# Kernel tuning notes

Hardware: AMD Instinct MI355X
Metric: run time of the kernel (lower is better)

Reference implementation:

```python
import jax, jax.numpy as jnp
import numpy as np

M_DIM = 1024
N_HEADS = 16
H_DIM = M_DIM // N_HEADS
B, S_DEC, S_ENC = 2, 2048, 2048
NEG = -1e9
LN_EPS = 1e-5


def _layernorm(x, g, b):
    mu = jnp.mean(x, axis=-1, keepdims=True)
    var = jnp.mean(jnp.square(x - mu), axis=-1, keepdims=True)
    return (x - mu) * jax.lax.rsqrt(var + LN_EPS) * g + b


def _mha(q_in, kv_in, Wq, bq, Wk, bk, Wv, bv, causal):
    # Wq/Wk/Wv: [H, m_dim, h_dim]; stacked equivalent of per-head nn.Linear
    q = jnp.einsum('bsm,hmd->bhsd', q_in, Wq) + bq[:, None, :]
    k = jnp.einsum('bsm,hmd->bhsd', kv_in, Wk) + bk[:, None, :]
    v = jnp.einsum('bsm,hmd->bhsd', kv_in, Wv) + bv[:, None, :]
    scores = jnp.einsum('bhqd,bhkd->bhqk', q, k) / jnp.sqrt(jnp.asarray(H_DIM, q.dtype))
    if causal:
        sq, sk = scores.shape[-2], scores.shape[-1]
        mask = jnp.tril(jnp.ones((sq, sk), dtype=bool))
        scores = jnp.where(mask, scores, jnp.asarray(NEG, scores.dtype))
    attn = jax.nn.softmax(scores, axis=-1)
    o = jnp.einsum('bhqk,bhkd->bhqd', attn, v)
    bsz, h, sq, d = o.shape
    # concat order: head-major along last dim, same as torch.cat over heads
    return o.transpose(0, 2, 1, 3).reshape(bsz, sq, h * d)


def setup_inputs() -> dict:
    key = jax.random.key(0)
    ks = jax.random.split(key, 32)
    s = 1.0 / np.sqrt(M_DIM)
    s2 = 1.0 / np.sqrt(2 * M_DIM)
    d = {
        'input': jax.random.normal(ks[0], (B, S_DEC, M_DIM), jnp.float32),
        'encoder_out': jax.random.normal(ks[1], (B, S_ENC, M_DIM), jnp.float32),
        # self-attention heads (stacked)
        'Wq1': jax.random.normal(ks[2], (N_HEADS, M_DIM, H_DIM), jnp.float32) * s,
        'bq1': jnp.zeros((N_HEADS, H_DIM), jnp.float32),
        'Wk1': jax.random.normal(ks[3], (N_HEADS, M_DIM, H_DIM), jnp.float32) * s,
        'bk1': jnp.zeros((N_HEADS, H_DIM), jnp.float32),
        'Wv1': jax.random.normal(ks[4], (N_HEADS, M_DIM, H_DIM), jnp.float32) * s,
        'bv1': jnp.zeros((N_HEADS, H_DIM), jnp.float32),
        'Wo1': jax.random.normal(ks[5], (M_DIM, M_DIM), jnp.float32) * s,
        'bo1': jnp.zeros((M_DIM,), jnp.float32),
        'ln1_g': jnp.ones((M_DIM,), jnp.float32),
        'ln1_b': jnp.zeros((M_DIM,), jnp.float32),
        # cross-attention heads (stacked)
        'Wq2': jax.random.normal(ks[6], (N_HEADS, M_DIM, H_DIM), jnp.float32) * s,
        'bq2': jnp.zeros((N_HEADS, H_DIM), jnp.float32),
        'Wk2': jax.random.normal(ks[7], (N_HEADS, M_DIM, H_DIM), jnp.float32) * s,
        'bk2': jnp.zeros((N_HEADS, H_DIM), jnp.float32),
        'Wv2': jax.random.normal(ks[8], (N_HEADS, M_DIM, H_DIM), jnp.float32) * s,
        'bv2': jnp.zeros((N_HEADS, H_DIM), jnp.float32),
        'Wo2': jax.random.normal(ks[9], (M_DIM, M_DIM), jnp.float32) * s,
        'bo2': jnp.zeros((M_DIM,), jnp.float32),
        'ln2_g': jnp.ones((M_DIM,), jnp.float32),
        'ln2_b': jnp.zeros((M_DIM,), jnp.float32),
        # FFN (expansion factor 2, per source)
        'W_ff1': jax.random.normal(ks[10], (M_DIM, 2 * M_DIM), jnp.float32) * s,
        'b_ff1': jnp.zeros((2 * M_DIM,), jnp.float32),
        'W_ff2': jax.random.normal(ks[11], (2 * M_DIM, M_DIM), jnp.float32) * s2,
        'b_ff2': jnp.zeros((M_DIM,), jnp.float32),
        'ln3_g': jnp.ones((M_DIM,), jnp.float32),
        'ln3_b': jnp.zeros((M_DIM,), jnp.float32),
    }
    return d


def reference(input, encoder_out,
              Wq1, bq1, Wk1, bk1, Wv1, bv1, Wo1, bo1, ln1_g, ln1_b,
              Wq2, bq2, Wk2, bk2, Wv2, bv2, Wo2, bo2, ln2_g, ln2_b,
              W_ff1, b_ff1, W_ff2, b_ff2, ln3_g, ln3_b):
    # masked self-attention (dropout = identity in eval)
    sa = _mha(input, input, Wq1, bq1, Wk1, bk1, Wv1, bv1, causal=True)
    sa = sa @ Wo1 + bo1
    out1 = _layernorm(sa + input, ln1_g, ln1_b)
    # cross-attention
    ca = _mha(out1, encoder_out, Wq2, bq2, Wk2, bk2, Wv2, bv2, causal=False)
    ca = ca @ Wo2 + bo2
    out1 = _layernorm(out1 + ca, ln2_g, ln2_b)
    # FFN
    ff = jax.nn.relu(out1 @ W_ff1 + b_ff1) @ W_ff2 + b_ff2
    out = _layernorm(ff + out1, ln3_g, ln3_b)
    return out
```

## Files before the change

kernel.cpp:

```cpp
#include <hip/hip_runtime.h>
#include <math.h>

#define B_ 2
#define S_ 2048
#define M_ 1024
#define H_ 16
#define D_ 64
#define R_ (B_*S_)

typedef __attribute__((ext_vector_type(8))) short short8v;
typedef __attribute__((ext_vector_type(4))) float float4v;
typedef __attribute__((ext_vector_type(16))) float float16v;

__device__ __forceinline__ float4 ld4(const float* p) {
    return *(const float4* __restrict__)p;
}

__device__ __forceinline__ ushort f2bf(float f) {
    union { float f; unsigned u; } x; x.f = f;
    unsigned u = x.u + 0x7fffu + ((x.u >> 16) & 1u);
    return (ushort)(u >> 16);
}
__device__ __forceinline__ float bf2f(ushort s) {
    union { unsigned u; float f; } x; x.u = ((unsigned)s) << 16; return x.f;
}
__device__ __forceinline__ unsigned cvtpk(float lo, float hi) {
    unsigned r;
    asm("v_cvt_pk_bf16_f32 %0, %1, %2" : "=v"(r) : "v"(lo), "v"(hi));
    return r;
}
#if __has_builtin(__builtin_amdgcn_exp2f)
__device__ __forceinline__ float fexp2(float x) { return __builtin_amdgcn_exp2f(x); }
#else
__device__ __forceinline__ float fexp2(float x) { return exp2f(x); }
#endif
#if __has_builtin(__builtin_amdgcn_rcpf)
__device__ __forceinline__ float frcp(float x) { return __builtin_amdgcn_rcpf(x); }
#else
__device__ __forceinline__ float frcp(float x) { return 1.f / x; }
#endif
__device__ __forceinline__ float4v mfma16(short8v a, short8v b, float4v c) {
    return __builtin_amdgcn_mfma_f32_16x16x32_bf16(a, b, c, 0, 0, 0);
}
__device__ __forceinline__ float16v mfma32(short8v a, short8v b, float16v c) {
    return __builtin_amdgcn_mfma_f32_32x32x16_bf16(a, b, c, 0, 0, 0);
}
__device__ __forceinline__ void glds16(const void* g, void* l) {
    __builtin_amdgcn_global_load_lds(
        (const __attribute__((address_space(1))) void*)g,
        (__attribute__((address_space(3))) void*)l, 16, 0, 0);
}

__global__ __launch_bounds__(256) void cast2_k(const float* __restrict__ a,
                                               const float* __restrict__ b,
                                               ushort* __restrict__ oa,
                                               ushort* __restrict__ ob) {
    size_t u = (size_t)blockIdx.x * 256 + threadIdx.x;
    const float* in; ushort* out;
    if (u < (1u << 20)) { in = a; out = oa; }
    else { u -= (1u << 20); in = b; out = ob; }
    float4 v = ld4(in + u * 4);
    ushort4 o = { f2bf(v.x), f2bf(v.y), f2bf(v.z), f2bf(v.w) };
    *(ushort4*)&out[u * 4] = o;
}

__global__ __launch_bounds__(256) void biasp_k(
    const float* __restrict__ q1, const float* __restrict__ k1,
    const float* __restrict__ v1, const float* __restrict__ k2,
    const float* __restrict__ v2, const float* __restrict__ q2,
    float* __restrict__ dst, float SCv) {
    const int seg = blockIdx.x >> 2;
    const int li = (blockIdx.x & 3) * 256 + threadIdx.x;
    const float* s; int off; float sc;
    switch (seg) {
        case 0: s = q1; off = 0;    sc = SCv; break;
        case 1: s = k1; off = 1024; sc = 1.f; break;
        case 2: s = v1; off = 2048; sc = 1.f; break;
        case 3: s = k2; off = 4096; sc = 1.f; break;
        case 4: s = v2; off = 5120; sc = 1.f; break;
        default: s = q2; off = 8192; sc = SCv; break;
    }
    dst[off + li] = s[li] * sc;
}

__global__ __launch_bounds__(256) void wtransH_k(
    const float* __restrict__ s0, const float* __restrict__ s1,
    const float* __restrict__ s2, const float* __restrict__ s3,
    const float* __restrict__ s4, const float* __restrict__ s5,
    ushort* __restrict__ oQKV1, ushort* __restrict__ oQ2,
    ushort* __restrict__ oKV2, float SCv) {
    __shared__ float t[32][33];
    const int z = blockIdx.z, s6 = z >> 4, h = z & 15;
    const float* srcs[6] = { s0, s1, s2, s3, s4, s5 };
    const float* ib = srcs[s6] + (size_t)h * 1024 * 64;
    ushort* ob;
    if (s6 < 3)       ob = oQKV1 + (size_t)s6 * (1024 * 1024) + (size_t)h * (64 * 1024);
    else if (s6 == 3) ob = oQ2 + (size_t)h * (64 * 1024);
    else              ob = oKV2 + (size_t)(s6 - 4) * (1024 * 1024) + (size_t)h * (64 * 1024);
    const float scale = (s6 == 0 || s6 == 3) ? SCv : 1.f;
    const int k0 = blockIdx.y * 32, n0 = blockIdx.x * 32;
    const int tx = threadIdx.x & 31, ty = threadIdx.x >> 5;
    #pragma unroll
    for (int i = 0; i < 4; ++i)
        t[ty + i * 8][tx] = ib[(size_t)(k0 + ty + i * 8) * 64 + n0 + tx];
    __syncthreads();
    #pragma unroll
    for (int i = 0; i < 4; ++i)
        ob[(size_t)(n0 + ty + i * 8) * 1024 + k0 + tx] = f2bf(t[tx][ty + i * 8] * scale);
}

__global__ __launch_bounds__(256) void wtrans_k(const float* __restrict__ inA,
                                                const float* __restrict__ inB,
                                                ushort* __restrict__ outA,
                                                ushort* __restrict__ outB,
                                                int K, int N) {
    __shared__ float t[32][33];
    const float* ib = blockIdx.z ? inB : inA;
    ushort* ob = blockIdx.z ? outB : outA;
    const int k0 = blockIdx.y * 32, n0 = blockIdx.x * 32;
    const int tx = threadIdx.x & 31, ty = threadIdx.x >> 5;
    #pragma unroll
    for (int i = 0; i < 4; ++i)
        t[ty + i * 8][tx] = ib[(size_t)(k0 + ty + i * 8) * N + n0 + tx];
    __syncthreads();
    #pragma unroll
    for (int i = 0; i < 4; ++i)
        ob[(size_t)(n0 + ty + i * 8) * K + k0 + tx] = f2bf(t[tx][ty + i * 8]);
}

template<int TM, int TN, int BK, int OUTMODE, int ACT>
__global__ __launch_bounds__(256) void gemm_bf16_k(
    const ushort* __restrict__ A, const ushort* __restrict__ Bt,
    const float* __restrict__ bias, void* __restrict__ C,
    ushort* __restrict__ Cvt, int matV, int N, int K)
{
    constexpr int NI = TM / 32;
    constexpr int NJ = TN / 32;
    constexpr int KS = BK / 32;
    constexpr int CHR = BK / 8;
    __shared__ __align__(16) ushort At[TM * BK];
    __shared__ __align__(16) ushort Bts[TN * BK];
    const int tid = threadIdx.x, lane = tid & 63, w = tid >> 6;
    const int wm = w >> 1, wn = w & 1;
    const int q = lane & 15, g = lane >> 4;
    const int m0 = blockIdx.y * TM, n0 = blockIdx.x * TN;

    float4v acc[NI][NJ];
    #pragma unroll
    for (int i = 0; i < NI; ++i)
        #pragma unroll
        for (int j = 0; j < NJ; ++j) acc[i][j] = (float4v){0.f, 0.f, 0.f, 0.f};

    for (int k0 = 0; k0 < K; k0 += BK) {
        #pragma unroll
        for (int t = 0; t < TM * CHR / 256; ++t) {
            const int cb = (w * (TM * CHR / 256) + t) * 64;
            const int c = cb + lane;
            const int row = c / CHR, kc = (c % CHR) ^ (row & (CHR - 1));
            glds16(&A[(size_t)(m0 + row) * K + k0 + kc * 8], &At[cb * 8]);
        }
        #pragma unroll
        for (int t = 0; t < TN * CHR / 256; ++t) {
            const int cb = (w * (TN * CHR / 256) + t) * 64;
            const int c = cb + lane;
            const int row = c / CHR, kc = (c % CHR) ^ (row & (CHR - 1));
            glds16(&Bt[(size_t)(n0 + row) * K + k0 + kc * 8], &Bts[cb * 8]);
        }
        __syncthreads();
        #pragma unroll
        for (int ks = 0; ks < KS; ++ks) {
            short8v af[NI], bf[NJ];
            #pragma unroll
            for (int i = 0; i < NI; ++i) {
                const int row = wm * (TM / 2) + i * 16 + q;
                af[i] = *(const short8v*)((const char*)At +
                        row * (BK * 2) + (((ks * 4 + g) ^ (q & (CHR - 1))) << 4));
            }
            #pragma unroll
            for (int j = 0; j < NJ; ++j) {
                const int row = wn * (TN / 2) + j * 16 + q;
                bf[j] = *(const short8v*)((const char*)Bts +
                        row * (BK * 2) + (((ks * 4 + g) ^ (q & (CHR - 1))) << 4));
            }
            #pragma unroll
            for (int i = 0; i < NI; ++i)
                #pragma unroll
                for (int j = 0; j < NJ; ++j)
                    acc[i][j] = mfma16(af[i], bf[j], acc[i][j]);
        }
        __syncthreads();
    }

    float bcol[NJ];
    #pragma unroll
    for (int j = 0; j < NJ; ++j) bcol[j] = bias[n0 + wn * (TN / 2) + j * 16 + q];

    #pragma unroll
    for (int i = 0; i < NI; ++i) {
        const int rowg0 = m0 + wm * (TM / 2) + i * 16 + g * 4;
        #pragma unroll
        for (int j = 0; j < NJ; ++j) {
            const int colg = n0 + wn * (TN / 2) + j * 16 + q;
            float v[4];
            #pragma unroll
            for (int r = 0; r < 4; ++r) {
                v[r] = acc[i][j][r] + bcol[j];
                if (ACT) v[r] = fmaxf(v[r], 0.f);
            }
            if (OUTMODE == 0) {
                #pragma unroll
                for (int r = 0; r < 4; ++r)
                    ((float*)C)[(size_t)(rowg0 + r) * N + colg] = v[r];
            } else if (OUTMODE == 1) {
                #pragma unroll
                for (int r = 0; r < 4; ++r)
                    ((ushort*)C)[(size_t)(rowg0 + r) * N + colg] = f2bf(v[r]);
            } else {
                const int mat = colg >> 10, h = (colg >> 6) & 15, d = colg & 63;
                const int bb = rowg0 >> 11, s0 = rowg0 & 2047;
                if (mat == matV) {
                    uint2 pv;
                    pv.x = cvtpk(v[0], v[1]);
                    pv.y = cvtpk(v[2], v[3]);
                    *(uint2*)&Cvt[((size_t)(bb * H_ + h) * D_ + d) * S_ + s0] = pv;
                } else {
                    #pragma unroll
                    for (int r = 0; r < 4; ++r)
                        ((ushort*)C)[((((size_t)(mat * B_ + bb) * H_ + h) * S_) + s0 + r) * D_ + d] = f2bf(v[r]);
                }
            }
        }
    }
}

template<int CAUSAL>
__global__ __launch_bounds__(256, 3) void fattn_k(
    const ushort* __restrict__ Qg, const ushort* __restrict__ Kg,
    const ushort* __restrict__ VTg, ushort* __restrict__ Og, int Skv)
{
    __shared__ __align__(16) ushort Kt[2][64 * 64];
    __shared__ __align__(16) ushort Vt[2][64 * 64];
    const int tid = threadIdx.x, lane = tid & 63, w = tid >> 6;
    const int q = lane & 31, hi = lane >> 5;
    const int id = blockIdx.x;
    const int bh = id & 31;
    const int t_ = id >> 5;
    const int qb = CAUSAL ? ((t_ < 8) ? (15 - t_) : (t_ - 8)) : t_;
    const int q0b = qb * 128;
    const int q0w = q0b + w * 32;
    const float MB = 24.f;

    const int c0 = tid, c1 = tid + 256;
    const ushort* kS0 = Kg + ((size_t)bh * Skv + (c0 >> 3)) * 64 + (((c0 & 7) ^ ((c0 >> 3) & 7)) * 8);
    const ushort* kS1 = Kg + ((size_t)bh * Skv + (c1 >> 3)) * 64 + (((c1 & 7) ^ ((c1 >> 3) & 7)) * 8);
    const ushort* vS0 = VTg + ((size_t)bh * 64 + (c0 >> 3)) * (size_t)Skv + (((c0 & 7) ^ ((c0 >> 3) & 7)) * 8);
    const ushort* vS1 = VTg + ((size_t)bh * 64 + (c1 >> 3)) * (size_t)Skv + (((c1 & 7) ^ ((c1 >> 3) & 7)) * 8);

#define STAGE(nb) do { \
        glds16(kS0, &Kt[nb][(w * 64) * 8]); \
        glds16(kS1, &Kt[nb][(256 + w * 64) * 8]); \
        glds16(vS0, &Vt[nb][(w * 64) * 8]); \
        glds16(vS1, &Vt[nb][(256 + w * 64) * 8]); \
        kS0 += 64 * 64; kS1 += 64 * 64; vS0 += 64; vS1 += 64; } while (0)

    short8v qf[4];
    #pragma unroll
    for (int ki = 0; ki < 4; ++ki)
        qf[ki] = *(const short8v*)&Qg[((size_t)bh * S_ + q0w + q) * 64 + ki * 16 + hi * 8];

    const int ktB = q * 128 + ((hi ^ (q & 7)) << 4);

    float16v oacc0, oacc1;
    #pragma unroll
    for (int r = 0; r < 16; ++r) { oacc0[r] = 0.f; oacc1[r] = 0.f; }
    float l_ = 0.f;

    const int ktiles = CAUSAL ? (2 * qb + 2) : (Skv >> 6);
    int cur = 0;

    STAGE(0);
    __syncthreads();

    for (int kt = 0; kt < ktiles; ++kt) {
        if (kt + 1 < ktiles) STAGE(cur ^ 1);
        const char* ktp = (const char*)Kt + cur * 8192;
        const char* vtp = (const char*)Vt + cur * 8192;
        const int kv0 = kt * 64;

        float16v st0, st1;
        #pragma unroll
        for (int r = 0; r < 16; ++r) { st0[r] = 0.f; st1[r] = 0.f; }
        __builtin_amdgcn_s_setprio(1);
        #pragma unroll
        for (int ki = 0; ki < 4; ++ki) {
            short8v kf0 = *(const short8v*)(ktp + (ktB ^ (ki << 5)));
            short8v kf1 = *(const short8v*)(ktp + (ktB ^ (ki << 5)) + 4096);
            st0 = mfma32(kf0, qf[ki], st0);
            st1 = mfma32(kf1, qf[ki], st1);
        }
        __builtin_amdgcn_s_setprio(0);

        if (CAUSAL && kv0 + 63 > q0b) {
            const int qg_ = q0w + q;
            #pragma unroll
            for (int r = 0; r < 16; ++r) {
                const int row = (r & 3) + 8 * (r >> 2) + 4 * hi;
                if (kv0 + row > qg_)      st0[r] = -1e9f;
                if (kv0 + 32 + row > qg_) st1[r] = -1e9f;
            }
        }

        float ts[16];
        #pragma unroll
        for (int r = 0; r < 16; ++r) {
            st0[r] = fexp2(st0[r] - MB);
            st1[r] = fexp2(st1[r] - MB);
            ts[r] = st0[r] + st1[r];
        }
        #pragma unroll
        for (int off = 8; off >= 1; off >>= 1)
            #pragma unroll
            for (int i = 0; i < 8; ++i)
                if (i < off) ts[i] += ts[i + off];
        l_ += ts[0] + __shfl_xor(ts[0], 32);

        unsigned W0[8], W1[8];
        #pragma unroll
        for (int s = 0; s < 8; ++s) {
            W0[s] = cvtpk(st0[2 * s], st0[2 * s + 1]);
            W1[s] = cvtpk(st1[2 * s], st1[2 * s + 1]);
        }

        short8v bq[4];
        #pragma unroll
        for (int kb = 0; kb < 4; ++kb) {
            union { unsigned u[4]; short8v v; } bb;
            #pragma unroll
            for (int j = 0; j < 4; ++j) {
                const unsigned* Wb = (kb >> 1) ? W1 : W0;
                const int s0 = (j & 1) + 4 * (kb & 1);
                const unsigned own  = hi ? Wb[s0 + 2] : Wb[s0];
                const unsigned send = hi ? Wb[s0]     : Wb[s0 + 2];
                const unsigned rec  = (unsigned)__shfl_xor((int)send, 32);
                bb.u[j] = (j >> 1) ? (hi ? own : rec) : (hi ? rec : own);
            }
            bq[kb] = bb.v;
        }

        __builtin_amdgcn_s_setprio(1);
        #pragma unroll
        for (int kb = 0; kb < 4; ++kb) {
            short8v vf0 = *(const short8v*)(vtp + (ktB ^ (kb << 5)));
            short8v vf1 = *(const short8v*)(vtp + (ktB ^ (kb << 5)) + 4096);
            oacc0 = mfma32(vf0, bq[kb], oacc0);
            oacc1 = mfma32(vf1, bq[kb], oacc1);
        }
        __builtin_amdgcn_s_setprio(0);

        __syncthreads();
        cur ^= 1;
    }
#undef STAGE

    float lr = l_ + __shfl_xor(l_, 32) - __shfl_xor(l_, 32);
    const float inv = frcp(l_);
    (void)lr;
    char* Ob = (char*)Kt;
    const int qr = w * 32 + q;
    #pragma unroll
    for (int s = 0; s < 8; ++s) {
        const int d0a = 2 * (s & 1) + 8 * (s >> 1) + 4 * hi;
        unsigned wa = cvtpk(oacc0[2 * s] * inv, oacc0[2 * s + 1] * inv);
        *(unsigned*)(Ob + qr * 128 + ((((d0a >> 3) ^ (qr & 7)) << 4) | ((2 * d0a) & 15))) = wa;
        const int d0b = d0a + 32;
        unsigned wb = cvtpk(oacc1[2 * s] * inv, oacc1[2 * s + 1] * inv);
        *(unsigned*)(Ob + qr * 128 + ((((d0b >> 3) ^ (qr & 7)) << 4) | ((2 * d0b) & 15))) = wb;
    }
    __syncthreads();
    const int b = bh >> 4, h = bh & 15;
    #pragma unroll
    for (int t = 0; t < 4; ++t) {
        const int c = t * 256 + tid;
        const int qrow = c >> 3, ch = c & 7;
        short8v v = *(const short8v*)(Ob + qrow * 128 + ((ch ^ (qrow & 7)) << 4));
        *(short8v*)&Og[((size_t)(b * S_ + q0b + qrow)) * M_ + h * 64 + ch * 8] = v;
    }
}

template<int EMITB>
__global__ __launch_bounds__(256) void ln_k(
    const ushort* __restrict__ X, const float* __restrict__ Rz,
    const float* __restrict__ g, const float* __restrict__ be,
    float* __restrict__ outf, ushort* __restrict__ outb)
{
    __shared__ float red[8];
    const int row = blockIdx.x, tid = threadIdx.x;
    const int lane = tid & 63, w = tid >> 6;

    ushort4 xu = *(const ushort4*)&X[(size_t)row * M_ + tid * 4];
    float4 rr = ld4(Rz + (size_t)row * M_ + tid * 4);
    float4 x = make_float4(bf2f(xu.x) + rr.x, bf2f(xu.y) + rr.y,
                           bf2f(xu.z) + rr.z, bf2f(xu.w) + rr.w);

    float sm = x.x + x.y + x.z + x.w;
    #pragma unroll
    for (int off = 1; off < 64; off <<= 1) sm += __shfl_xor(sm, off);
    if (lane == 0) red[w] = sm;
    __syncthreads();
    const float mean = (red[0] + red[1] + red[2] + red[3]) * (1.f / M_);

    x.x -= mean; x.y -= mean; x.z -= mean; x.w -= mean;
    float vs = x.x * x.x + x.y * x.y + x.z * x.z + x.w * x.w;
    #pragma unroll
    for (int off = 1; off < 64; off <<= 1) vs += __shfl_xor(vs, off);
    if (lane == 0) red[4 + w] = vs;
    __syncthreads();
    const float var = (red[4] + red[5] + red[6] + red[7]) * (1.f / M_);
    const float rs = rsqrtf(var + 1e-5f);

    float4 gg = ld4(g + tid * 4), bb = ld4(be + tid * 4);
    float4 y = make_float4(x.x * rs * gg.x + bb.x, x.y * rs * gg.y + bb.y,
                           x.z * rs * gg.z + bb.z, x.w * rs * gg.w + bb.w);
    *(float4*)(outf + (size_t)row * M_ + tid * 4) = y;
    if (EMITB) {
        ushort4 ob = { f2bf(y.x), f2bf(y.y), f2bf(y.z), f2bf(y.w) };
        *(ushort4*)&outb[(size_t)row * M_ + tid * 4] = ob;
    }
}

extern "C" void kernel_launch(void* const* d_in, const int* in_sizes, int n_in,
                              void* d_out, int out_size, void* d_ws, size_t ws_size,
                              hipStream_t stream)
{
    const float* input = (const float*)d_in[0];
    const float* enc   = (const float*)d_in[1];
    const float* Wq1 = (const float*)d_in[2];  const float* bq1 = (const float*)d_in[3];
    const float* Wk1 = (const float*)d_in[4];  const float* bk1 = (const float*)d_in[5];
    const float* Wv1 = (const float*)d_in[6];  const float* bv1 = (const float*)d_in[7];
    const float* Wo1 = (const float*)d_in[8];  const float* bo1 = (const float*)d_in[9];
    const float* ln1g = (const float*)d_in[10]; const float* ln1b = (const float*)d_in[11];
    const float* Wq2 = (const float*)d_in[12]; const float* bq2 = (const float*)d_in[13];
    const float* Wk2 = (const float*)d_in[14]; const float* bk2 = (const float*)d_in[15];
    const float* Wv2 = (const float*)d_in[16]; const float* bv2 = (const float*)d_in[17];
    const float* Wo2 = (const float*)d_in[18]; const float* bo2 = (const float*)d_in[19];
    const float* ln2g = (const float*)d_in[20]; const float* ln2b = (const float*)d_in[21];
    const float* Wf1 = (const float*)d_in[22]; const float* bf1 = (const float*)d_in[23];
    const float* Wf2 = (const float*)d_in[24]; const float* bf2 = (const float*)d_in[25];
    const float* ln3g = (const float*)d_in[26]; const float* ln3b = (const float*)d_in[27];

    const float SC = 0.18033688011112042f;

    char* W = (char*)d_ws;
    #define OFS(mb) ((void*)(W + (size_t)(mb) * 1024 * 1024))
    ushort* x0b    = (ushort*)OFS(0);
    ushort* encb   = (ushort*)OFS(8);
    ushort* WqkvT1 = (ushort*)OFS(16);
    ushort* Wo1T   = (ushort*)OFS(22);
    ushort* Wq2T   = (ushort*)OFS(24);
    ushort* WkvT2  = (ushort*)OFS(26);
    ushort* Wo2T   = (ushort*)OFS(30);
    ushort* Wf1T   = (ushort*)OFS(32);
    ushort* Wf2T   = (ushort*)OFS(36);
    float*  biasQKV1 = (float*)OFS(40);
    float*  biasKV2  = (float*)((char*)OFS(40) + 16384);
    float*  biasQ2   = (float*)((char*)OFS(40) + 32768);
    ushort* QKV1   = (ushort*)OFS(41);
    ushort* VT1    = (ushort*)OFS(65);
    ushort* att1b  = (ushort*)OFS(73);
    ushort* o1b    = (ushort*)OFS(81);
    float*  out1f  = (float*)OFS(41);
    ushort* out1b  = (ushort*)OFS(57);
    ushort* Q2     = (ushort*)OFS(65);
    ushort* KV2    = (ushort*)OFS(73);
    ushort* VT2    = (ushort*)OFS(0);
    ushort* att2b  = (ushort*)OFS(8);
    ushort* o2b    = (ushort*)OFS(65);
    float*  out2f  = (float*)OFS(73);
    ushort* out2b  = (ushort*)OFS(0);
    ushort* ff1b   = (ushort*)OFS(41);
    ushort* ff2b   = (ushort*)OFS(57);
    float*  out    = (float*)d_out;
    const size_t MAT = (size_t)B_ * H_ * S_ * D_;

    dim3 blk(256);

    cast2_k<<<8192, blk, 0, stream>>>(input, enc, x0b, encb);
    biasp_k<<<24, blk, 0, stream>>>(bq1, bk1, bv1, bk2, bv2, bq2, biasQKV1, SC);
    wtransH_k<<<dim3(2, 32, 96), blk, 0, stream>>>(Wq1, Wk1, Wv1, Wq2, Wk2, Wv2,
                                                   WqkvT1, Wq2T, WkvT2, SC);
    wtrans_k<<<dim3(32, 32, 2), blk, 0, stream>>>(Wo1, Wo2, Wo1T, Wo2T, 1024, 1024);
    wtrans_k<<<dim3(64, 32, 1), blk, 0, stream>>>(Wf1, Wf1, Wf1T, Wf1T, 1024, 2048);
    wtrans_k<<<dim3(32, 64, 1), blk, 0, stream>>>(Wf2, Wf2, Wf2T, Wf2T, 2048, 1024);

    gemm_bf16_k<128, 128, 64, 2, 0><<<dim3(24, 32), blk, 0, stream>>>(
        x0b, WqkvT1, biasQKV1, QKV1, VT1, 2, 3072, 1024);
    fattn_k<1><<<dim3(512), blk, 0, stream>>>(QKV1, QKV1 + MAT, VT1, att1b, S_);
    gemm_bf16_k<64, 64, 64, 1, 0><<<dim3(16, 64), blk, 0, stream>>>(
        att1b, Wo1T, bo1, o1b, nullptr, 9, 1024, 1024);
    ln_k<1><<<dim3(R_), blk, 0, stream>>>(o1b, input, ln1g, ln1b, out1f, out1b);

    gemm_bf16_k<64, 64, 64, 2, 0><<<dim3(16, 64), blk, 0, stream>>>(
        out1b, Wq2T, biasQ2, Q2, nullptr, 9, 1024, 1024);
    gemm_bf16_k<128, 128, 64, 2, 0><<<dim3(16, 32), blk, 0, stream>>>(
        encb, WkvT2, biasKV2, KV2, VT2, 1, 2048, 1024);
    fattn_k<0><<<dim3(512), blk, 0, stream>>>(Q2, KV2, VT2, att2b, S_);
    gemm_bf16_k<64, 64, 64, 1, 0><<<dim3(16, 64), blk, 0, stream>>>(
        att2b, Wo2T, bo2, o2b, nullptr, 9, 1024, 1024);
    ln_k<1><<<dim3(R_), blk, 0, stream>>>(o2b, out1f, ln2g, ln2b, out2f, out2b);

    gemm_bf16_k<128, 64, 64, 1, 1><<<dim3(32, 32), blk, 0, stream>>>(
        out2b, Wf1T, bf1, ff1b, nullptr, 9, 2048, 1024);
    gemm_bf16_k<64, 64, 64, 1, 0><<<dim3(16, 64), blk, 0, stream>>>(
        ff1b, Wf2T, bf2, ff2b, nullptr, 9, 1024, 2048);
    ln_k<0><<<dim3(R_), blk, 0, stream>>>(ff2b, out2f, ln3g, ln3b, out, nullptr);
    #undef OFS
}
```

Measured before the change: 302.1 us.

## Halve attention query tile to 64 rows with 128-thread blocks

The flash-attention kernel now uses 2 wavefronts per block covering 64 query rows instead of 4 wavefronts covering 128, doubling the grid to 1024 blocks. The causal query-block ordering is remapped to interleave long and short blocks, and only the final KV tile gets masked. Smaller blocks are meant to improve load balance and CU occupancy, with finer causal skipping. In exchange, each K/V tile staged into shared memory is reused by half as many queries, which doubles K/V load traffic.

Result: slower. 328.3 us (+8.7%).

```diff
diff --git a/kernel.cpp b/kernel.cpp
--- a/kernel.cpp
+++ b/kernel.cpp
@@ -234,7 +234,7 @@
 }
 
 template<int CAUSAL>
-__global__ __launch_bounds__(256, 3) void fattn_k(
+__global__ __launch_bounds__(128) void fattn_k(
     const ushort* __restrict__ Qg, const ushort* __restrict__ Kg,
     const ushort* __restrict__ VTg, ushort* __restrict__ Og, int Skv)
 {
@@ -245,23 +245,37 @@
     const int id = blockIdx.x;
     const int bh = id & 31;
     const int t_ = id >> 5;
-    const int qb = CAUSAL ? ((t_ < 8) ? (15 - t_) : (t_ - 8)) : t_;
-    const int q0b = qb * 128;
+    int qb;
+    if (CAUSAL) {
+        if (t_ < 8)       qb = 31 - t_;
+        else if (t_ < 16) qb = t_ - 8;
+        else if (t_ < 24) qb = 39 - t_;
+        else              qb = t_ - 16;
+    } else qb = t_;
+    const int q0b = qb * 64;
     const int q0w = q0b + w * 32;
     const float MB = 24.f;
 
-    const int c0 = tid, c1 = tid + 256;
-    const ushort* kS0 = Kg + ((size_t)bh * Skv + (c0 >> 3)) * 64 + (((c0 & 7) ^ ((c0 >> 3) & 7)) * 8);
-    const ushort* kS1 = Kg + ((size_t)bh * Skv + (c1 >> 3)) * 64 + (((c1 & 7) ^ ((c1 >> 3) & 7)) * 8);
-    const ushort* vS0 = VTg + ((size_t)bh * 64 + (c0 >> 3)) * (size_t)Skv + (((c0 & 7) ^ ((c0 >> 3) & 7)) * 8);
-    const ushort* vS1 = VTg + ((size_t)bh * 64 + (c1 >> 3)) * (size_t)Skv + (((c1 & 7) ^ ((c1 >> 3) & 7)) * 8);
+    const ushort* kS[4]; const ushort* vS[4];
+    #pragma unroll
+    for (int i = 0; i < 4; ++i) {
+        const int c = i * 128 + tid;
+        const int r = c >> 3, ch = c & 7, sc = ch ^ (r & 7);
+        kS[i] = Kg + ((size_t)bh * Skv + r) * 64 + sc * 8;
+        vS[i] = VTg + ((size_t)bh * 64 + r) * (size_t)Skv + sc * 8;
+    }
 
 #define STAGE(nb) do { \
-        glds16(kS0, &Kt[nb][(w * 64) * 8]); \
-        glds16(kS1, &Kt[nb][(256 + w * 64) * 8]); \
-        glds16(vS0, &Vt[nb][(w * 64) * 8]); \
-        glds16(vS1, &Vt[nb][(256 + w * 64) * 8]); \
-        kS0 += 64 * 64; kS1 += 64 * 64; vS0 += 64; vS1 += 64; } while (0)
+        glds16(kS[0], &Kt[nb][(tid) * 8]); \
+        glds16(kS[1], &Kt[nb][(tid + 128) * 8]); \
+        glds16(kS[2], &Kt[nb][(tid + 256) * 8]); \
+        glds16(kS[3], &Kt[nb][(tid + 384) * 8]); \
+        glds16(vS[0], &Vt[nb][(tid) * 8]); \
+        glds16(vS[1], &Vt[nb][(tid + 128) * 8]); \
+        glds16(vS[2], &Vt[nb][(tid + 256) * 8]); \
+        glds16(vS[3], &Vt[nb][(tid + 384) * 8]); \
+        kS[0] += 64 * 64; kS[1] += 64 * 64; kS[2] += 64 * 64; kS[3] += 64 * 64; \
+        vS[0] += 64; vS[1] += 64; vS[2] += 64; vS[3] += 64; } while (0)
 
     short8v qf[4];
     #pragma unroll
@@ -275,7 +289,7 @@
     for (int r = 0; r < 16; ++r) { oacc0[r] = 0.f; oacc1[r] = 0.f; }
     float l_ = 0.f;
 
-    const int ktiles = CAUSAL ? (2 * qb + 2) : (Skv >> 6);
+    const int ktiles = CAUSAL ? (qb + 1) : (Skv >> 6);
     int cur = 0;
 
     STAGE(0);
@@ -300,7 +314,7 @@
         }
         __builtin_amdgcn_s_setprio(0);
 
-        if (CAUSAL && kv0 + 63 > q0b) {
+        if (CAUSAL && kt == ktiles - 1) {
             const int qg_ = q0w + q;
             #pragma unroll
             for (int r = 0; r < 16; ++r) {
@@ -362,9 +376,7 @@
     }
 #undef STAGE
 
-    float lr = l_ + __shfl_xor(l_, 32) - __shfl_xor(l_, 32);
     const float inv = frcp(l_);
-    (void)lr;
     char* Ob = (char*)Kt;
     const int qr = w * 32 + q;
     #pragma unroll
@@ -380,7 +392,7 @@
     const int b = bh >> 4, h = bh & 15;
     #pragma unroll
     for (int t = 0; t < 4; ++t) {
-        const int c = t * 256 + tid;
+        const int c = t * 128 + tid;
         const int qrow = c >> 3, ch = c & 7;
         short8v v = *(const short8v*)(Ob + qrow * 128 + ((ch ^ (qrow & 7)) << 4));
         *(short8v*)&Og[((size_t)(b * S_ + q0b + qrow)) * M_ + h * 64 + ch * 8] = v;
@@ -483,6 +495,7 @@
     const size_t MAT = (size_t)B_ * H_ * S_ * D_;
 
     dim3 blk(256);
+    dim3 blkA(128);
 
     cast2_k<<<8192, blk, 0, stream>>>(input, enc, x0b, encb);
     biasp_k<<<24, blk, 0, stream>>>(bq1, bk1, bv1, bk2, bv2, bq2, biasQKV1, SC);
@@ -494,7 +507,7 @@
 
     gemm_bf16_k<128, 128, 64, 2, 0><<<dim3(24, 32), blk, 0, stream>>>(
         x0b, WqkvT1, biasQKV1, QKV1, VT1, 2, 3072, 1024);
-    fattn_k<1><<<dim3(512), blk, 0, stream>>>(QKV1, QKV1 + MAT, VT1, att1b, S_);
+    fattn_k<1><<<dim3(1024), blkA, 0, stream>>>(QKV1, QKV1 + MAT, VT1, att1b, S_);
     gemm_bf16_k<64, 64, 64, 1, 0><<<dim3(16, 64), blk, 0, stream>>>(
         att1b, Wo1T, bo1, o1b, nullptr, 9, 1024, 1024);
     ln_k<1><<<dim3(R_), blk, 0, stream>>>(o1b, input, ln1g, ln1b, out1f, out1b);
@@ -503,7 +516,7 @@
         out1b, Wq2T, biasQ2, Q2, nullptr, 9, 1024, 1024);
     gemm_bf16_k<128, 128, 64, 2, 0><<<dim3(16, 32), blk, 0, stream>>>(
         encb, WkvT2, biasKV2, KV2, VT2, 1, 2048, 1024);
-    fattn_k<0><<<dim3(512), blk, 0, stream>>>(Q2, KV2, VT2, att2b, S_);
+    fattn_k<0><<<dim3(1024), blkA, 0, stream>>>(Q2, KV2, VT2, att2b, S_);
     gemm_bf16_k<64, 64, 64, 1, 0><<<dim3(16, 64), blk, 0, stream>>>(
         att2b, Wo2T, bo2, o2b, nullptr, 9, 1024, 1024);
     ln_k<1><<<dim3(R_), blk, 0, stream>>>(o2b, out1f, ln2g, ln2b, out2f, out2b);
```
